# Kernel tuning notes

Measured on AMD Instinct MI355X. Metric: run time of the kernel, lower is better.

The kernel has to match this reference:

```python
import jax, jax.numpy as jnp
import numpy as np

NB, H = 4, 16
EPS = 1e-5


def _ln(x, w=None, b=None):
    m = jnp.mean(x, -1, keepdims=True)
    v = jnp.var(x, -1, keepdims=True)
    y = (x - m) * jax.lax.rsqrt(v + EPS)
    if w is not None:
        y = y * w
    if b is not None:
        y = y + b
    return y


def _ada_ln(a, s, ln_s_w, w_gamma, w_beta):
    # AF3 Algorithm 26: a <- sigmoid(Lin(LN_nobias(s))) * LN_noaffine(a) + Lin(LN_nobias(s))
    a_n = _ln(a)
    s_n = _ln(s, ln_s_w)
    return jax.nn.sigmoid(s_n @ w_gamma) * a_n + s_n @ w_beta


def setup_inputs():
    key = jax.random.key(0)
    B, S, c_a, c_s, c_z = 1, 1024, 768, 384, 128
    n_hidden = 2 * c_a  # expansion factor n=2
    ks = iter(jax.random.split(key, 40))

    def rn(shape, scale=1.0):
        return scale * jax.random.normal(next(ks), shape, dtype=jnp.float32)

    p = 0.02
    return {
        "a": rn((B, S, c_a)),
        "s": rn((B, S, c_s)),
        "z": rn((B, S, S, c_z)),
        "beta": rn((B, S, S, H)),
        # per-block AttentionPairBias params (stacked over NB blocks)
        "ln_s_w_attn": jnp.ones((NB, c_s)),
        "wg_attn": rn((NB, c_s, c_a), p),
        "wb_attn": rn((NB, c_s, c_a), p),
        "wq": rn((NB, c_a, c_a), p),
        "bq": jnp.zeros((NB, c_a)),
        "wk": rn((NB, c_a, c_a), p),
        "wv": rn((NB, c_a, c_a), p),
        "ln_z_w": jnp.ones((NB, c_z)),
        "ln_z_b": jnp.zeros((NB, c_z)),
        "wpb": rn((NB, c_z, H), p),
        "wgate": rn((NB, c_a, c_a), p),
        "wo": rn((NB, c_a, c_a), p),
        "wsg_attn": rn((NB, c_s, c_a), p),
        "bsg_attn": -2.0 * jnp.ones((NB, c_a)),
        # per-block ConditionedTransitionBlock params
        "ln_s_w_tr": jnp.ones((NB, c_s)),
        "wg_tr": rn((NB, c_s, c_a), p),
        "wb_tr": rn((NB, c_s, c_a), p),
        "w_swish": rn((NB, c_a, n_hidden), p),
        "w_gate2": rn((NB, c_a, n_hidden), p),
        "wsg_tr": rn((NB, c_s, c_a), p),
        "bsg_tr": -2.0 * jnp.ones((NB, c_a)),
        "w_out": rn((NB, n_hidden, c_a), p),
    }


def reference(a, s, z, beta, ln_s_w_attn, wg_attn, wb_attn, wq, bq, wk, wv,
              ln_z_w, ln_z_b, wpb, wgate, wo, wsg_attn, bsg_attn,
              ln_s_w_tr, wg_tr, wb_tr, w_swish, w_gate2, wsg_tr, bsg_tr, w_out):
    B, S, c_a = a.shape
    d = c_a // H
    scale = 1.0 / jnp.sqrt(jnp.float32(d))
    for i in range(NB):
        # --- AttentionPairBias (AF3 Alg 24) ---
        ah = _ada_ln(a, s, ln_s_w_attn[i], wg_attn[i], wb_attn[i])
        q = (ah @ wq[i] + bq[i]).reshape(B, S, H, d)
        k = (ah @ wk[i]).reshape(B, S, H, d)
        v = (ah @ wv[i]).reshape(B, S, H, d)
        zb = _ln(z, ln_z_w[i], ln_z_b[i]) @ wpb[i]  # [B,S,S,H] pair bias
        scores = jnp.einsum('bihd,bjhd->bhij', q, k) * scale \
                 + jnp.transpose(zb + beta, (0, 3, 1, 2))
        attn = jax.nn.softmax(scores, axis=-1)
        o = jnp.einsum('bhij,bjhd->bihd', attn, v)
        g = jax.nn.sigmoid(ah @ wgate[i]).reshape(B, S, H, d)
        att_out = (g * o).reshape(B, S, c_a) @ wo[i]
        b_attn = jax.nn.sigmoid(s @ wsg_attn[i] + bsg_attn[i]) * att_out
        # --- ConditionedTransitionBlock (AF3 Alg 25, SwiGLU) ---
        th = _ada_ln(a, s, ln_s_w_tr[i], wg_tr[i], wb_tr[i])
        hidden = jax.nn.silu(th @ w_swish[i]) * (th @ w_gate2[i])
        tr = jax.nn.sigmoid(s @ wsg_tr[i] + bsg_tr[i]) * (hidden @ w_out[i])
        a = b_attn + tr
    return a
```

## Files before the change

kernel.cpp:

```cpp
#include <hip/hip_runtime.h>
#include <hip/hip_bf16.h>

typedef __hip_bfloat16 bf16;
typedef __attribute__((ext_vector_type(8))) short s8v;
typedef __attribute__((ext_vector_type(4))) float f4v;

constexpr int S = 1024, CA = 768, CS = 384, CZ = 128, NHID = 1536;
constexpr int NBLK = 4, NHEAD = 16, DH = 48;
constexpr float EPS = 1e-5f;

#define DEV static __device__ __forceinline__

DEV float sigmoidf_(float x) { return 1.0f / (1.0f + __expf(-x)); }

DEV f4v mfma16(s8v a, s8v b, f4v c) {
  return __builtin_amdgcn_mfma_f32_16x16x32_bf16(a, b, c, 0, 0, 0);
}

union U8 { s8v s; bf16 h[8]; };
union U4 { uint2 u; bf16 h[4]; };

DEV float wred_sum(float v) {
#pragma unroll
  for (int o = 32; o; o >>= 1) v += __shfl_xor(v, o);
  return v;
}

struct PrepFatArgs {
  const float* tsrc[14];
  bf16* tdst[14];
  const float* tcs[14];
  long tdstZ[14];
  const float *ln_z_w, *ln_z_b, *wpb, *bq, *bsg_a, *bsg_t;
  bf16* W2T; float* bias2; float* biasQKVG; float* biasSG;
  const float* s_in; bf16* s_hat; bf16* s_bf;
};

__global__ __launch_bounds__(256) void prep_fat(PrepFatArgs a) {
  __shared__ __align__(16) float tile[1056];
  const int bid = blockIdx.x, t = threadIdx.x;
  if (bid < 32256) {
    int ti, blk, x, y, K, N;
    if (bid < 6912) {
      const int lb = bid; ti = lb / 1152; const int r2 = lb % 1152;
      blk = r2 / 288; const int rem = r2 % 288; x = rem % 24; y = rem / 24; K = 384; N = 768;
    } else if (bid < 18432) {
      const int lb = bid - 6912; ti = 6 + lb / 2304; const int r2 = lb % 2304;
      blk = r2 / 576; const int rem = r2 % 576; x = rem % 24; y = rem / 24; K = 768; N = 768;
    } else if (bid < 27648) {
      const int lb = bid - 18432; ti = 11 + lb / 4608; const int r2 = lb % 4608;
      blk = r2 / 1152; const int rem = r2 % 1152; x = rem % 48; y = rem / 48; K = 768; N = 1536;
    } else {
      const int lb = bid - 27648; ti = 13; blk = lb / 1152;
      const int rem = lb % 1152; x = rem % 24; y = rem / 24; K = 1536; N = 768;
    }
    const float* src = a.tsrc[ti] + (size_t)blk * K * N;
    bf16* dst = a.tdst[ti] + (size_t)blk * a.tdstZ[ti];
    const float* cs = a.tcs[ti] ? (a.tcs[ti] + blk * CS) : nullptr;
    const int k0 = y * 32, n0 = x * 32, tx = t & 31, ty = t >> 5;
#pragma unroll
    for (int q = 0; q < 4; ++q) {
      const int k = k0 + ty + 8 * q;
      float v = src[(size_t)k * N + n0 + tx];
      if (cs) v *= cs[k];
      tile[(ty + 8 * q) * 33 + tx] = v;
    }
    __syncthreads();
#pragma unroll
    for (int q = 0; q < 4; ++q)
      dst[(size_t)(n0 + ty + 8 * q) * K + k0 + tx] = __float2bfloat16(tile[tx * 33 + ty + 8 * q]);
    return;
  }
  if (bid < 32305) {
    const int pid = bid - 32256;
    if (pid == 48) {
      for (int f = t; f < 64 * CZ; f += 256) {
        const int col = f >> 7, c = f & 127, b = col >> 4, h = col & 15;
        a.W2T[f] = __float2bfloat16(a.ln_z_w[b * CZ + c] * a.wpb[(b * CZ + c) * NHEAD + h]);
      }
      if (t < 64) {
        const int b = t >> 4, h = t & 15;
        float sum = 0.f;
        for (int c = 0; c < CZ; ++c)
          sum += a.ln_z_b[b * CZ + c] * a.wpb[(b * CZ + c) * NHEAD + h];
        a.bias2[t] = sum;
      }
      return;
    }
    const int g = pid * 256 + t;
    if (g < 4 * 3072) {
      const int b = g / 3072, c = g % 3072;
      a.biasQKVG[g] = (c < 768) ? a.bq[b * 768 + c] : 0.f;
    }
    if (g < 6144) {
      const int b = g / 1536, c = g % 1536;
      a.biasSG[g] = (c < 768) ? a.bsg_a[b * 768 + c] : a.bsg_t[b * 768 + c - 768];
    }
    return;
  }
  {
    float* red = tile;
    const size_t row = bid - 32305;
    float4 v = make_float4(0.f, 0.f, 0.f, 0.f);
    if (t < CS / 4) v = ((const float4*)(a.s_in + row * CS))[t];
    float sum = v.x + v.y + v.z + v.w;
    float sq = v.x * v.x + v.y * v.y + v.z * v.z + v.w * v.w;
    sum = wred_sum(sum); sq = wred_sum(sq);
    const int wv = t >> 6;
    if ((t & 63) == 0) { red[2 * wv] = sum; red[2 * wv + 1] = sq; }
    __syncthreads();
    sum = red[0] + red[2] + red[4] + red[6];
    sq = red[1] + red[3] + red[5] + red[7];
    const float m = sum / CS;
    const float rstd = rsqrtf(sq / CS - m * m + EPS);
    if (t < CS / 4) {
      U4 oh, ob_;
      oh.h[0] = __float2bfloat16((v.x - m) * rstd); oh.h[1] = __float2bfloat16((v.y - m) * rstd);
      oh.h[2] = __float2bfloat16((v.z - m) * rstd); oh.h[3] = __float2bfloat16((v.w - m) * rstd);
      ob_.h[0] = __float2bfloat16(v.x); ob_.h[1] = __float2bfloat16(v.y);
      ob_.h[2] = __float2bfloat16(v.z); ob_.h[3] = __float2bfloat16(v.w);
      *(uint2*)(a.s_hat + row * CS + 4 * t) = oh.u;
      *(uint2*)(a.s_bf + row * CS + 4 * t) = ob_.u;
    }
  }
}

__global__ __launch_bounds__(256) void ln_adaln2(const float* __restrict__ a,
                                                 const bf16* __restrict__ ada,
                                                 bf16* __restrict__ ah_attn,
                                                 bf16* __restrict__ ah_tr) {
  __shared__ float red[8];
  const int t = threadIdx.x;
  const size_t row = blockIdx.x;
  float4 v = make_float4(0.f, 0.f, 0.f, 0.f);
  if (t < 192) v = ((const float4*)(a + row * CA))[t];
  float sum = v.x + v.y + v.z + v.w;
  float sq = v.x * v.x + v.y * v.y + v.z * v.z + v.w * v.w;
  sum = wred_sum(sum); sq = wred_sum(sq);
  const int wv = t >> 6;
  if ((t & 63) == 0) { red[2 * wv] = sum; red[2 * wv + 1] = sq; }
  __syncthreads();
  sum = red[0] + red[2] + red[4] + red[6];
  sq = red[1] + red[3] + red[5] + red[7];
  const float m = sum / CA;
  const float rstd = rsqrtf(sq / CA - m * m + EPS);
  if (t < 192) {
    const float an[4] = {(v.x - m) * rstd, (v.y - m) * rstd, (v.z - m) * rstd, (v.w - m) * rstd};
    const bf16* ar = ada + row * 12288 + 4 * t;
    U4 g1, b1, g2, b2, o1, o2;
    g1.u = *(const uint2*)(ar);
    b1.u = *(const uint2*)(ar + 768);
    g2.u = *(const uint2*)(ar + 1536);
    b2.u = *(const uint2*)(ar + 2304);
#pragma unroll
    for (int j = 0; j < 4; ++j) {
      o1.h[j] = __float2bfloat16(sigmoidf_(__bfloat162float(g1.h[j])) * an[j] + __bfloat162float(b1.h[j]));
      o2.h[j] = __float2bfloat16(sigmoidf_(__bfloat162float(g2.h[j])) * an[j] + __bfloat162float(b2.h[j]));
    }
    *(uint2*)(ah_attn + row * CA + 4 * t) = o1.u;
    *(uint2*)(ah_tr + row * CA + 4 * t) = o2.u;
  }
}

__global__ __launch_bounds__(256) void final_adaln(const float* __restrict__ sg,
                                                   const bf16* __restrict__ att,
                                                   const bf16* __restrict__ tr,
                                                   const bf16* __restrict__ ada,
                                                   bf16* __restrict__ ah_attn,
                                                   bf16* __restrict__ ah_tr) {
  __shared__ float red[8];
  const int t = threadIdx.x;
  const size_t row = blockIdx.x;
  float o[4] = {0.f, 0.f, 0.f, 0.f};
  if (t < 192) {
    const float4 sa = *(const float4*)(sg + row * 6144 + 4 * t);
    const float4 st = *(const float4*)(sg + row * 6144 + 768 + 4 * t);
    U4 av, tv;
    av.u = *(const uint2*)(att + row * CA + 4 * t);
    tv.u = *(const uint2*)(tr + row * CA + 4 * t);
    o[0] = sa.x * __bfloat162float(av.h[0]) + st.x * __bfloat162float(tv.h[0]);
    o[1] = sa.y * __bfloat162float(av.h[1]) + st.y * __bfloat162float(tv.h[1]);
    o[2] = sa.z * __bfloat162float(av.h[2]) + st.z * __bfloat162float(tv.h[2]);
    o[3] = sa.w * __bfloat162float(av.h[3]) + st.w * __bfloat162float(tv.h[3]);
  }
  float sum = o[0] + o[1] + o[2] + o[3];
  float sq = o[0] * o[0] + o[1] * o[1] + o[2] * o[2] + o[3] * o[3];
  sum = wred_sum(sum); sq = wred_sum(sq);
  const int wv = t >> 6;
  if ((t & 63) == 0) { red[2 * wv] = sum; red[2 * wv + 1] = sq; }
  __syncthreads();
  sum = red[0] + red[2] + red[4] + red[6];
  sq = red[1] + red[3] + red[5] + red[7];
  const float m = sum / CA;
  const float rstd = rsqrtf(sq / CA - m * m + EPS);
  if (t < 192) {
    const bf16* ar = ada + row * 12288 + 4 * t;
    U4 g1, b1, g2, b2, o1, o2;
    g1.u = *(const uint2*)(ar);
    b1.u = *(const uint2*)(ar + 768);
    g2.u = *(const uint2*)(ar + 1536);
    b2.u = *(const uint2*)(ar + 2304);
#pragma unroll
    for (int j = 0; j < 4; ++j) {
      const float an = (o[j] - m) * rstd;
      o1.h[j] = __float2bfloat16(sigmoidf_(__bfloat162float(g1.h[j])) * an + __bfloat162float(b1.h[j]));
      o2.h[j] = __float2bfloat16(sigmoidf_(__bfloat162float(g2.h[j])) * an + __bfloat162float(b2.h[j]));
    }
    *(uint2*)(ah_attn + row * CA + 4 * t) = o1.u;
    *(uint2*)(ah_tr + row * CA + 4 * t) = o2.u;
  }
}

__global__ __launch_bounds__(256) void ew_final(const float* __restrict__ sg,
                                                const bf16* __restrict__ att,
                                                const bf16* __restrict__ tr,
                                                float* __restrict__ out) {
  const int i = blockIdx.x * 256 + threadIdx.x;
  const int row = i / 192, col = (i % 192) * 4;
  const float4 sa = *(const float4*)(sg + (size_t)row * 6144 + col);
  const float4 st = *(const float4*)(sg + (size_t)row * 6144 + 768 + col);
  U4 av, tv;
  av.u = *(const uint2*)(att + (size_t)row * CA + col);
  tv.u = *(const uint2*)(tr + (size_t)row * CA + col);
  float4 o;
  o.x = sa.x * __bfloat162float(av.h[0]) + st.x * __bfloat162float(tv.h[0]);
  o.y = sa.y * __bfloat162float(av.h[1]) + st.y * __bfloat162float(tv.h[1]);
  o.z = sa.z * __bfloat162float(av.h[2]) + st.z * __bfloat162float(tv.h[2]);
  o.w = sa.w * __bfloat162float(av.h[3]) + st.w * __bfloat162float(tv.h[3]);
  *(float4*)(out + (size_t)row * CA + col) = o;
}

__global__ __launch_bounds__(256) void zbias_kernel(const float* __restrict__ z,
                                                    const float* __restrict__ beta,
                                                    const bf16* __restrict__ W2T,
                                                    const float* __restrict__ bias2,
                                                    bf16* __restrict__ bias_all) {
  __shared__ s8v zt8[64 * 16];
  __shared__ s8v w2s[64 * 16];
  __shared__ float betas[64][17];
  __shared__ float bias2s[64];
  __shared__ bf16 obuf[64][72];
  const int t = threadIdx.x;
  const int i = blockIdx.y, j0 = blockIdx.x * 64;
#pragma unroll
  for (int q = 0; q < 4; ++q) {
    const int u = q * 256 + t;
    const int row = u >> 4, sl = u & 15;
    w2s[row * 16 + (sl ^ (row & 7))] = *(const s8v*)(W2T + row * CZ + sl * 8);
  }
  if (t < 64) bias2s[t] = bias2[t];
  {
    const int j = t >> 2, h4 = t & 3;
    const float4 bv = *(const float4*)(beta + ((size_t)i * S + j0 + j) * NHEAD + 4 * h4);
    betas[j][4 * h4 + 0] = bv.x; betas[j][4 * h4 + 1] = bv.y;
    betas[j][4 * h4 + 2] = bv.z; betas[j][4 * h4 + 3] = bv.w;
  }
  {
    const int p = t >> 2, q = t & 3;
    const float* zr = z + ((size_t)i * S + j0 + p) * CZ + q * 32;
    float vals[32];
    float sum = 0.f, sq = 0.f;
#pragma unroll
    for (int k4 = 0; k4 < 8; ++k4) {
      const float4 xv = *(const float4*)(zr + 4 * k4);
      vals[4 * k4 + 0] = xv.x; vals[4 * k4 + 1] = xv.y;
      vals[4 * k4 + 2] = xv.z; vals[4 * k4 + 3] = xv.w;
      sum += xv.x + xv.y + xv.z + xv.w;
      sq += xv.x * xv.x + xv.y * xv.y + xv.z * xv.z + xv.w * xv.w;
    }
    sum += __shfl_xor(sum, 1); sum += __shfl_xor(sum, 2);
    sq += __shfl_xor(sq, 1); sq += __shfl_xor(sq, 2);
    const float m = sum / CZ;
    const float rstd = rsqrtf(sq / CZ - m * m + EPS);
#pragma unroll
    for (int u = 0; u < 4; ++u) {
      U8 pk;
#pragma unroll
      for (int e = 0; e < 8; ++e) pk.h[e] = __float2bfloat16((vals[8 * u + e] - m) * rstd);
      const int cu = 4 * q + u;
      zt8[p * 16 + (cu ^ (p & 7))] = pk.s;
    }
  }
  __syncthreads();
  const int lane = t & 63, wid = t >> 6;
  const int wr = wid >> 1, wc = wid & 1;
  const int ln = lane & 15, lq = lane >> 4;
  f4v acc[2][2] = {};
#pragma unroll
  for (int kk = 0; kk < 4; ++kk) {
    const int sl = (lq + 4 * kk) ^ (ln & 7);
    s8v a[2], b[2];
#pragma unroll
    for (int mi = 0; mi < 2; ++mi) a[mi] = zt8[(32 * wr + 16 * mi + ln) * 16 + sl];
#pragma unroll
    for (int ni = 0; ni < 2; ++ni) b[ni] = w2s[(32 * wc + 16 * ni + ln) * 16 + sl];
#pragma unroll
    for (int mi = 0; mi < 2; ++mi)
#pragma unroll
      for (int ni = 0; ni < 2; ++ni) acc[mi][ni] = mfma16(a[mi], b[ni], acc[mi][ni]);
  }
#pragma unroll
  for (int mi = 0; mi < 2; ++mi)
#pragma unroll
    for (int ni = 0; ni < 2; ++ni) {
      const int col = 32 * wc + 16 * ni + ln;
      const int jb = 32 * wr + 16 * mi + 4 * lq;
      U4 o4;
#pragma unroll
      for (int r = 0; r < 4; ++r)
        o4.h[r] = __float2bfloat16(acc[mi][ni][r] + bias2s[col] + betas[jb + r][col & 15]);
      *(uint2*)&obuf[col][jb] = o4.u;
    }
  __syncthreads();
  {
    const int oc = t >> 2, js = (t & 3) * 16;
    bf16* dp = bias_all + (size_t)oc * S * S + (size_t)i * S + j0 + js;
    *(s8v*)dp = *(const s8v*)&obuf[oc][js];
    *(s8v*)(dp + 8) = *(const s8v*)&obuf[oc][js + 8];
  }
}

struct GemmAArgs {
  const bf16* A0[2]; int lda0[2];
  const bf16* A1[2]; int lda1[2];
  const bf16* Bt[2];
  const float* bias[2];
  void* C[2];
  int K[2]; int N[2]; int nb[2];
  int amode[2]; int outMode[2];
  bf16* vT;
};

DEV s8v combineRT(s8v x, s8v y, int amode) {
  U8 ux, uy, rr;
  ux.s = x; uy.s = y;
#pragma unroll
  for (int j = 0; j < 8; ++j) {
    const float fx = __bfloat162float(ux.h[j]);
    const float fy = __bfloat162float(uy.h[j]);
    const float tt = sigmoidf_(fx);
    rr.h[j] = __float2bfloat16((amode == 2 ? fx * tt : tt) * fy);
  }
  return rr.s;
}

__global__ __launch_bounds__(256) void gemmA(GemmAArgs ga) {
  const int z = blockIdx.z;
  if ((int)blockIdx.x >= ga.nb[z]) return;
  __shared__ s8v As[512];
  __shared__ s8v Bs[1024];
  const bf16* A0 = ga.A0[z]; const int lda0 = ga.lda0[z];
  const bf16* A1 = ga.A1[z]; const int lda1 = ga.lda1[z];
  const bf16* Bt = ga.Bt[z];
  const float* bias = ga.bias[z];
  const int K = ga.K[z], N = ga.N[z], amode = ga.amode[z], om = ga.outMode[z];
  const int t = threadIdx.x;
  const int lane = t & 63, wid = t >> 6;
  const int wr = wid >> 1, wc = wid & 1;
  const int ln = lane & 15, lq = lane >> 4;
  const int m0 = blockIdx.y * 64, n0 = blockIdx.x * 128;
  int rowA[2], slA[2], swzA[2];
#pragma unroll
  for (int q = 0; q < 2; ++q) {
    const int u = q * 256 + t;
    rowA[q] = u >> 3; slA[q] = u & 7;
    swzA[q] = rowA[q] * 8 + (slA[q] ^ (rowA[q] & 7));
  }
  int rowB[4], slB[4], swzB[4];
#pragma unroll
  for (int q = 0; q < 4; ++q) {
    const int u = q * 256 + t;
    rowB[q] = u >> 3; slB[q] = u & 7;
    swzB[q] = rowB[q] * 8 + (slB[q] ^ (rowB[q] & 7));
  }
  f4v acc[2][4] = {};
  s8v ra[2], ra2[2], rb[4];
#pragma unroll
  for (int q = 0; q < 2; ++q) {
    ra[q] = *(const s8v*)(A0 + (size_t)(m0 + rowA[q]) * lda0 + slA[q] * 8);
    if (amode != 0) ra2[q] = *(const s8v*)(A1 + (size_t)(m0 + rowA[q]) * lda1 + slA[q] * 8);
  }
#pragma unroll
  for (int q = 0; q < 4; ++q)
    rb[q] = *(const s8v*)(Bt + (size_t)(n0 + rowB[q]) * K + slB[q] * 8);
  for (int ks = 0;;) {
    __syncthreads();
#pragma unroll
    for (int q = 0; q < 2; ++q)
      As[swzA[q]] = (amode == 0) ? ra[q] : combineRT(ra[q], ra2[q], amode);
#pragma unroll
    for (int q = 0; q < 4; ++q) Bs[swzB[q]] = rb[q];
    const int ksn = ks + 64;
    if (ksn < K) {
#pragma unroll
      for (int q = 0; q < 2; ++q) {
        ra[q] = *(const s8v*)(A0 + (size_t)(m0 + rowA[q]) * lda0 + ksn + slA[q] * 8);
        if (amode != 0) ra2[q] = *(const s8v*)(A1 + (size_t)(m0 + rowA[q]) * lda1 + ksn + slA[q] * 8);
      }
#pragma unroll
      for (int q = 0; q < 4; ++q)
        rb[q] = *(const s8v*)(Bt + (size_t)(n0 + rowB[q]) * K + ksn + slB[q] * 8);
    }
    __syncthreads();
#pragma unroll
    for (int kk = 0; kk < 2; ++kk) {
      const int sl = (lq + 4 * kk) ^ (ln & 7);
      s8v a[2], b[4];
#pragma unroll
      for (int mi = 0; mi < 2; ++mi) a[mi] = As[(32 * wr + 16 * mi + ln) * 8 + sl];
#pragma unroll
      for (int ni = 0; ni < 4; ++ni) b[ni] = Bs[(64 * wc + 16 * ni + ln) * 8 + sl];
#pragma unroll
      for (int mi = 0; mi < 2; ++mi)
#pragma unroll
        for (int ni = 0; ni < 4; ++ni) acc[mi][ni] = mfma16(a[mi], b[ni], acc[mi][ni]);
    }
    ks = ksn;
    if (ks >= K) break;
  }
  const bool vdiv = (ga.vT != nullptr) && (z == 0) && (n0 >= 1536) && (n0 < 2304);
#pragma unroll
  for (int ni = 0; ni < 4; ++ni) {
    const int n = n0 + 64 * wc + 16 * ni + ln;
    const float bv = bias ? bias[n] : 0.f;
#pragma unroll
    for (int mi = 0; mi < 2; ++mi) {
      const int mb = m0 + 32 * wr + 16 * mi + 4 * lq;
      if (vdiv) {
        U4 o4;
#pragma unroll
        for (int r = 0; r < 4; ++r) o4.h[r] = __float2bfloat16(acc[mi][ni][r] + bv);
        *(uint2*)(ga.vT + (size_t)(n - 1536) * S + mb) = o4.u;
      } else if (om == 0) {
        bf16* Cb = (bf16*)ga.C[z];
#pragma unroll
        for (int r = 0; r < 4; ++r)
          Cb[(size_t)(mb + r) * N + n] = __float2bfloat16(acc[mi][ni][r] + bv);
      } else {
        float* Cf = (float*)ga.C[z];
#pragma unroll
        for (int r = 0; r < 4; ++r)
          Cf[(size_t)(mb + r) * N + n] = sigmoidf_(acc[mi][ni][r] + bv);
      }
    }
  }
}

__global__ __launch_bounds__(256) void flash_split(const bf16* __restrict__ qkvg,
                                                   const bf16* __restrict__ vT,
                                                   const bf16* __restrict__ bias_all,
                                                   float* __restrict__ opart,
                                                   float* __restrict__ ml, int blk) {
  __shared__ s8v Qs[64 * 8];
  __shared__ s8v Ks[64 * 8];
  __shared__ s8v Vs[48 * 8];
  __shared__ s8v Bs[64 * 8];
  __shared__ bf16 PwB[4 * 1024];
  __shared__ float facL[4][16];
  const int t = threadIdx.x;
  const int lane = t & 63, w = t >> 6;
  const int ln = lane & 15, lq = lane >> 4;
  const int h = blockIdx.y, i0 = blockIdx.x * 64, part = blockIdx.z;
  const bf16* bp = bias_all + (size_t)(blk * NHEAD + h) * S * S;
  const float scale = 0.14433756729740643f;

#pragma unroll
  for (int uu = 0; uu < 2; ++uu) {
    const int u = t + 256 * uu, row = u >> 3, sl = u & 7;
    s8v qv{};
    if (sl < 6) qv = *(const s8v*)(qkvg + (size_t)(i0 + row) * 3072 + h * DH + sl * 8);
    Qs[row * 8 + (sl ^ (row & 7))] = qv;
  }

  s8v kr[2], br[2], vr0{}, vr1{};
  auto prefetch = [&](int jt) {
    const int j0 = jt * 64;
#pragma unroll
    for (int uu = 0; uu < 2; ++uu) {
      const int u = t + 256 * uu, row = u >> 3, sl = u & 7;
      s8v kv{};
      if (sl < 6) kv = *(const s8v*)(qkvg + (size_t)(j0 + row) * 3072 + 768 + h * DH + sl * 8);
      kr[uu] = kv;
      br[uu] = *(const s8v*)(bp + (size_t)(i0 + row) * S + j0 + sl * 8);
    }
    { const int d = t >> 3, sl = t & 7;
      vr0 = *(const s8v*)(vT + (size_t)(h * DH + d) * S + j0 + sl * 8); }
    if (t < 128) {
      const int u = 256 + t, d = u >> 3, sl = u & 7;
      vr1 = *(const s8v*)(vT + (size_t)(h * DH + d) * S + j0 + sl * 8);
    }
  };
  auto store_tiles = [&]() {
#pragma unroll
    for (int uu = 0; uu < 2; ++uu) {
      const int u = t + 256 * uu, row = u >> 3, sl = u & 7;
      const int ph = row * 8 + (sl ^ (row & 7));
      Ks[ph] = kr[uu];
      Bs[ph] = br[uu];
    }
    { const int d = t >> 3, sl = t & 7;
      Vs[d * 8 + (sl ^ (d & 7))] = vr0; }
    if (t < 128) {
      const int u = 256 + t, d = u >> 3, sl = u & 7;
      Vs[d * 8 + (sl ^ (d & 7))] = vr1;
    }
  };

  float m_run = -3e30f, l_run = 0.f;
  f4v acc_o[3] = {};
  bf16* pw = PwB + w * 1024;

  prefetch(part * 4);
  for (int jt2 = 0; jt2 < 4; ++jt2) {
    __syncthreads();
    store_tiles();
    __syncthreads();
    if (jt2 < 3) prefetch(part * 4 + jt2 + 1);
    float p[4][4];
    float tmax = -3e30f;
    __builtin_amdgcn_s_setprio(1);
#pragma unroll
    for (int ja = 0; ja < 4; ++ja) {
      f4v accs = {};
#pragma unroll
      for (int ks2 = 0; ks2 < 2; ++ks2) {
        const int sl = (lq + 4 * ks2) ^ (ln & 7);
        const s8v a = Ks[(16 * ja + ln) * 8 + sl];
        const s8v b = Qs[(16 * w + ln) * 8 + sl];
        accs = mfma16(a, b, accs);
      }
      const int jq = 4 * ja + lq;
      const int pu = jq >> 1;
      U4 bv;
      bv.u = *(const uint2*)((const bf16*)(&Bs[0]) +
                             (((16 * w + ln) * 8 + (pu ^ (ln & 7))) * 8 + (jq & 1) * 4));
#pragma unroll
      for (int r = 0; r < 4; ++r) {
        p[ja][r] = accs[r] * scale + __bfloat162float(bv.h[r]);
        tmax = fmaxf(tmax, p[ja][r]);
      }
    }
    __builtin_amdgcn_s_setprio(0);
    tmax = fmaxf(tmax, __shfl_xor(tmax, 16));
    tmax = fmaxf(tmax, __shfl_xor(tmax, 32));
    const float m_new = fmaxf(m_run, tmax);
    const float fac = __expf(m_run - m_new);
    m_run = m_new;
    float psum = 0.f;
#pragma unroll
    for (int ja = 0; ja < 4; ++ja)
#pragma unroll
      for (int r = 0; r < 4; ++r) {
        p[ja][r] = __expf(p[ja][r] - m_new);
        psum += p[ja][r];
      }
    psum += __shfl_xor(psum, 16);
    psum += __shfl_xor(psum, 32);
    l_run = l_run * fac + psum;
    if (lq == 0) facL[w][ln] = fac;
#pragma unroll
    for (int ja = 0; ja < 4; ++ja) {
      const int ju = 4 * ja + lq;
      const int ph = ju ^ ((ln & 7) << 1);
      U4 pk;
#pragma unroll
      for (int r = 0; r < 4; ++r) pk.h[r] = __float2bfloat16(p[ja][r]);
      *(uint2*)(pw + ln * 64 + ph * 4) = pk.u;
    }
    asm volatile("s_waitcnt lgkmcnt(0)" ::: "memory");
    __builtin_amdgcn_sched_barrier(0);
    const float4 fv = *(const float4*)&facL[w][4 * lq];
#pragma unroll
    for (int ni = 0; ni < 3; ++ni) {
      acc_o[ni][0] *= fv.x; acc_o[ni][1] *= fv.y;
      acc_o[ni][2] *= fv.z; acc_o[ni][3] *= fv.w;
    }
    __builtin_amdgcn_s_setprio(1);
#pragma unroll
    for (int ks2 = 0; ks2 < 2; ++ks2) {
      const int pu0 = (2 * lq + 8 * ks2) ^ ((ln & 7) << 1);
      const s8v pa = *(const s8v*)(pw + ln * 64 + pu0 * 4);
      const int slv = (lq + 4 * ks2) ^ (ln & 7);
#pragma unroll
      for (int ni = 0; ni < 3; ++ni) {
        const s8v vb = Vs[(16 * ni + ln) * 8 + slv];
        acc_o[ni] = mfma16(pa, vb, acc_o[ni]);
      }
    }
    __builtin_amdgcn_s_setprio(0);
  }
  if (lq == 0) {
    ((float2*)ml)[(size_t)(part * NHEAD + h) * S + i0 + 16 * w + ln] =
        make_float2(m_run, l_run);
  }
  float* op = opart + (size_t)part * S * CA;
#pragma unroll
  for (int ni = 0; ni < 3; ++ni)
#pragma unroll
    for (int r = 0; r < 4; ++r) {
      const int m = i0 + 16 * w + 4 * lq + r;
      op[(size_t)m * CA + h * DH + 16 * ni + ln] = acc_o[ni][r];
    }
}

__global__ __launch_bounds__(256) void flash_combine4(const float* __restrict__ opart,
                                                      const float* __restrict__ ml,
                                                      const bf16* __restrict__ gate,
                                                      bf16* __restrict__ go) {
  const int row = blockIdx.x, t = threadIdx.x;
  if (t >= 192) return;
  const int c = 4 * t, h = t / 12;
  const float2* mlp = (const float2*)ml;
  const float2 a0 = mlp[(size_t)(0 * NHEAD + h) * S + row];
  const float2 a1 = mlp[(size_t)(1 * NHEAD + h) * S + row];
  const float2 a2 = mlp[(size_t)(2 * NHEAD + h) * S + row];
  const float2 a3 = mlp[(size_t)(3 * NHEAD + h) * S + row];
  const float M = fmaxf(fmaxf(a0.x, a1.x), fmaxf(a2.x, a3.x));
  const float w0 = __expf(a0.x - M), w1 = __expf(a1.x - M);
  const float w2 = __expf(a2.x - M), w3 = __expf(a3.x - M);
  const float inv = 1.0f / (w0 * a0.y + w1 * a1.y + w2 * a2.y + w3 * a3.y);
  const size_t rc = (size_t)row * CA + c;
  const float4 o0 = *(const float4*)(opart + rc);
  const float4 o1 = *(const float4*)(opart + (size_t)S * CA + rc);
  const float4 o2 = *(const float4*)(opart + (size_t)2 * S * CA + rc);
  const float4 o3 = *(const float4*)(opart + (size_t)3 * S * CA + rc);
  U4 g;
  g.u = *(const uint2*)(gate + (size_t)row * 3072 + c);
  U4 o;
  o.h[0] = __float2bfloat16(sigmoidf_(__bfloat162float(g.h[0])) *
                            ((w0 * o0.x + w1 * o1.x + w2 * o2.x + w3 * o3.x) * inv));
  o.h[1] = __float2bfloat16(sigmoidf_(__bfloat162float(g.h[1])) *
                            ((w0 * o0.y + w1 * o1.y + w2 * o2.y + w3 * o3.y) * inv));
  o.h[2] = __float2bfloat16(sigmoidf_(__bfloat162float(g.h[2])) *
                            ((w0 * o0.z + w1 * o1.z + w2 * o2.z + w3 * o3.z) * inv));
  o.h[3] = __float2bfloat16(sigmoidf_(__bfloat162float(g.h[3])) *
                            ((w0 * o0.w + w1 * o1.w + w2 * o2.w + w3 * o3.w) * inv));
  *(uint2*)(go + (size_t)row * CA + c) = o.u;
}

__global__ void fill_kernel(float* p, int n, float v) {
  const int i = blockIdx.x * 256 + threadIdx.x;
  if (i < n) p[i] = v;
}

extern "C" void kernel_launch(void* const* d_in, const int* in_sizes, int n_in,
                              void* d_out, int out_size, void* d_ws, size_t ws_size,
                              hipStream_t stream) {
  (void)in_sizes; (void)n_in;
  const float* a_in = (const float*)d_in[0];
  const float* s_in = (const float*)d_in[1];
  const float* z_in = (const float*)d_in[2];
  const float* beta = (const float*)d_in[3];
  const float* ln_s_w_attn = (const float*)d_in[4];
  const float* wg_attn = (const float*)d_in[5];
  const float* wb_attn = (const float*)d_in[6];
  const float* wq = (const float*)d_in[7];
  const float* bq = (const float*)d_in[8];
  const float* wk = (const float*)d_in[9];
  const float* wv = (const float*)d_in[10];
  const float* ln_z_w = (const float*)d_in[11];
  const float* ln_z_b = (const float*)d_in[12];
  const float* wpb = (const float*)d_in[13];
  const float* wgate = (const float*)d_in[14];
  const float* wo = (const float*)d_in[15];
  const float* wsg_attn = (const float*)d_in[16];
  const float* bsg_attn = (const float*)d_in[17];
  const float* ln_s_w_tr = (const float*)d_in[18];
  const float* wg_tr = (const float*)d_in[19];
  const float* wb_tr = (const float*)d_in[20];
  const float* w_swish = (const float*)d_in[21];
  const float* w_gate2 = (const float*)d_in[22];
  const float* wsg_tr = (const float*)d_in[23];
  const float* bsg_tr = (const float*)d_in[24];
  const float* w_out = (const float*)d_in[25];

  char* wp = (char*)d_ws;
  size_t used = 0;
  auto alloc = [&](size_t bytes) -> void* {
    void* p = wp + used;
    used += (bytes + 255) & ~(size_t)255;
    return p;
  };
  bf16* bias_all = (bf16*)alloc((size_t)64 * S * S * 2);
  bf16* WT_ada = (bf16*)alloc((size_t)4 * 3072 * 384 * 2);
  bf16* WT_sg = (bf16*)alloc((size_t)4 * 1536 * 384 * 2);
  bf16* WT_qkvg = (bf16*)alloc((size_t)4 * 3072 * 768 * 2);
  bf16* WT_wo = (bf16*)alloc((size_t)4 * 768 * 768 * 2);
  bf16* WT_mlp = (bf16*)alloc((size_t)4 * 3072 * 768 * 2);
  bf16* WT_wout = (bf16*)alloc((size_t)4 * 768 * 1536 * 2);
  float* biasQKVG = (float*)alloc(4 * 3072 * 4);
  float* biasSG = (float*)alloc(6144 * 4);
  bf16* W2T = (bf16*)alloc(64 * 128 * 2);
  float* bias2 = (float*)alloc(64 * 4);
  bf16* ada_all = (bf16*)alloc((size_t)S * 12288 * 2);
  float* sg_all = (float*)alloc((size_t)S * 6144 * 4);
  bf16* s_hat = (bf16*)alloc((size_t)S * CS * 2);
  bf16* s_bf = (bf16*)alloc((size_t)S * CS * 2);
  bf16* ah_attn = (bf16*)alloc((size_t)S * CA * 2);
  bf16* ah_tr = (bf16*)alloc((size_t)S * CA * 2);
  bf16* qkvg = (bf16*)alloc((size_t)S * 3072 * 2);
  bf16* vT = (bf16*)alloc((size_t)CA * S * 2);
  bf16* go = (bf16*)alloc((size_t)S * CA * 2);
  bf16* att = (bf16*)alloc((size_t)S * CA * 2);
  bf16* swg = (bf16*)alloc((size_t)S * 3072 * 2);
  bf16* trout = (bf16*)alloc((size_t)S * CA * 2);
  float* opart = (float*)alloc((size_t)4 * S * CA * 4);
  float* ml = (float*)alloc((size_t)4 * NHEAD * S * 8);
  if (used > ws_size) {
    fill_kernel<<<(out_size + 255) / 256, 256, 0, stream>>>((float*)d_out, out_size, 12345.0f);
    return;
  }

  const dim3 B256(256);

  {
    PrepFatArgs pa{};
    pa.tsrc[0] = wg_attn;  pa.tdst[0] = WT_ada + (size_t)0 * 384;    pa.tcs[0] = ln_s_w_attn; pa.tdstZ[0] = 3072 * 384;
    pa.tsrc[1] = wb_attn;  pa.tdst[1] = WT_ada + (size_t)768 * 384;  pa.tcs[1] = ln_s_w_attn; pa.tdstZ[1] = 3072 * 384;
    pa.tsrc[2] = wg_tr;    pa.tdst[2] = WT_ada + (size_t)1536 * 384; pa.tcs[2] = ln_s_w_tr;   pa.tdstZ[2] = 3072 * 384;
    pa.tsrc[3] = wb_tr;    pa.tdst[3] = WT_ada + (size_t)2304 * 384; pa.tcs[3] = ln_s_w_tr;   pa.tdstZ[3] = 3072 * 384;
    pa.tsrc[4] = wsg_attn; pa.tdst[4] = WT_sg + (size_t)0 * 384;     pa.tcs[4] = nullptr;     pa.tdstZ[4] = 1536 * 384;
    pa.tsrc[5] = wsg_tr;   pa.tdst[5] = WT_sg + (size_t)768 * 384;   pa.tcs[5] = nullptr;     pa.tdstZ[5] = 1536 * 384;
    pa.tsrc[6] = wq;    pa.tdst[6] = WT_qkvg + (size_t)0 * 768;    pa.tdstZ[6] = 3072 * 768;
    pa.tsrc[7] = wk;    pa.tdst[7] = WT_qkvg + (size_t)768 * 768;  pa.tdstZ[7] = 3072 * 768;
    pa.tsrc[8] = wv;    pa.tdst[8] = WT_qkvg + (size_t)1536 * 768; pa.tdstZ[8] = 3072 * 768;
    pa.tsrc[9] = wgate; pa.tdst[9] = WT_qkvg + (size_t)2304 * 768; pa.tdstZ[9] = 3072 * 768;
    pa.tsrc[10] = wo;   pa.tdst[10] = WT_wo;                       pa.tdstZ[10] = 768 * 768;
    pa.tsrc[11] = w_swish; pa.tdst[11] = WT_mlp + (size_t)0 * 768;    pa.tdstZ[11] = 3072 * 768;
    pa.tsrc[12] = w_gate2; pa.tdst[12] = WT_mlp + (size_t)1536 * 768; pa.tdstZ[12] = 3072 * 768;
    pa.tsrc[13] = w_out; pa.tdst[13] = WT_wout; pa.tdstZ[13] = 768 * 1536;
    pa.ln_z_w = ln_z_w; pa.ln_z_b = ln_z_b; pa.wpb = wpb;
    pa.bq = bq; pa.bsg_a = bsg_attn; pa.bsg_t = bsg_tr;
    pa.W2T = W2T; pa.bias2 = bias2; pa.biasQKVG = biasQKVG; pa.biasSG = biasSG;
    pa.s_in = s_in; pa.s_hat = s_hat; pa.s_bf = s_bf;
    prep_fat<<<33329, B256, 0, stream>>>(pa);
  }

  zbias_kernel<<<dim3(16, 1024), B256, 0, stream>>>(z_in, beta, W2T, bias2, bias_all);

  {
    GemmAArgs ga{};
    ga.A0[0] = s_hat; ga.lda0[0] = 384; ga.Bt[0] = WT_ada; ga.bias[0] = nullptr;
    ga.C[0] = ada_all; ga.K[0] = 384; ga.N[0] = 12288; ga.nb[0] = 96;
    ga.amode[0] = 0; ga.outMode[0] = 0;
    ga.A0[1] = s_bf; ga.lda0[1] = 384; ga.Bt[1] = WT_sg; ga.bias[1] = biasSG;
    ga.C[1] = sg_all; ga.K[1] = 384; ga.N[1] = 6144; ga.nb[1] = 48;
    ga.amode[1] = 0; ga.outMode[1] = 1;
    ga.vT = nullptr;
    gemmA<<<dim3(96, 16, 2), B256, 0, stream>>>(ga);
  }

  ln_adaln2<<<S, B256, 0, stream>>>(a_in, ada_all, ah_attn, ah_tr);
  for (int b = 0; b < NBLK; ++b) {
    {
      GemmAArgs ga{};
      ga.A0[0] = ah_attn; ga.lda0[0] = 768; ga.Bt[0] = WT_qkvg + (size_t)b * 3072 * 768;
      ga.bias[0] = biasQKVG + b * 3072; ga.C[0] = qkvg; ga.K[0] = 768; ga.N[0] = 3072;
      ga.nb[0] = 24; ga.amode[0] = 0; ga.outMode[0] = 0;
      ga.A0[1] = ah_tr; ga.lda0[1] = 768; ga.Bt[1] = WT_mlp + (size_t)b * 3072 * 768;
      ga.bias[1] = nullptr; ga.C[1] = swg; ga.K[1] = 768; ga.N[1] = 3072;
      ga.nb[1] = 24; ga.amode[1] = 0; ga.outMode[1] = 0;
      ga.vT = vT;
      gemmA<<<dim3(24, 16, 2), B256, 0, stream>>>(ga);
    }
    flash_split<<<dim3(16, 16, 4), B256, 0, stream>>>(qkvg, vT, bias_all, opart, ml, b);
    flash_combine4<<<S, B256, 0, stream>>>(opart, ml, qkvg + 2304, go);
    {
      GemmAArgs ga{};
      ga.A0[0] = go; ga.lda0[0] = 768;
      ga.Bt[0] = WT_wo + (size_t)b * 768 * 768; ga.bias[0] = nullptr;
      ga.C[0] = att; ga.K[0] = 768; ga.N[0] = 768; ga.nb[0] = 6;
      ga.amode[0] = 0; ga.outMode[0] = 0;
      ga.A0[1] = swg; ga.lda0[1] = 3072; ga.A1[1] = swg + 1536; ga.lda1[1] = 3072;
      ga.Bt[1] = WT_wout + (size_t)b * 768 * 1536; ga.bias[1] = nullptr;
      ga.C[1] = trout; ga.K[1] = 1536; ga.N[1] = 768; ga.nb[1] = 6;
      ga.amode[1] = 2; ga.outMode[1] = 0;
      ga.vT = nullptr;
      gemmA<<<dim3(6, 16, 2), B256, 0, stream>>>(ga);
    }
    if (b < NBLK - 1) {
      final_adaln<<<S, B256, 0, stream>>>(sg_all + (size_t)b * 1536, att, trout,
                                          ada_all + (size_t)(b + 1) * 3072, ah_attn, ah_tr);
    } else {
      ew_final<<<768, B256, 0, stream>>>(sg_all + (size_t)b * 1536, att, trout, (float*)d_out);
    }
  }
}
```

Baseline: 581.5 us.

## Fuse flash split-combine and gating into output-projection GEMM; halve KV splits

Splits the flash attention key range into 2 parts instead of 4, so each block processes 8 key tiles, and double-buffers the K/V/bias LDS tiles. The separate flash_combine4 kernel is removed. The output-projection GEMM now merges the two partial outputs and applies the sigmoid gate while loading its A tiles (amode 3). This removes one launch, the go intermediate and half of the partial-output traffic. In exchange the flash grid is half the size, and the A operand of the projection GEMM is loaded synchronously with scalar fp32 reads and recomputed by each of the 6 N-blocks.

```diff
diff --git a/kernel.cpp b/kernel.cpp
--- a/kernel.cpp
+++ b/kernel.cpp
@@ -329,6 +329,9 @@
   int K[2]; int N[2]; int nb[2];
   int amode[2]; int outMode[2];
   bf16* vT;
+  const float* opA;
+  const float* mlA;
+  const bf16* gateA;
 };
 
 DEV s8v combineRT(s8v x, s8v y, int amode) {
@@ -342,6 +345,26 @@
     rr.h[j] = __float2bfloat16((amode == 2 ? fx * tt : tt) * fy);
   }
   return rr.s;
+}
+
+DEV s8v combineFlash(const float* opart, const float* ml, const bf16* gate,
+                     int row, int k) {
+  const int h = k / DH;
+  const float2 m1 = ((const float2*)ml)[(size_t)h * S + row];
+  const float2 m2 = ((const float2*)ml)[(size_t)(NHEAD + h) * S + row];
+  const float M = fmaxf(m1.x, m2.x);
+  const float w1 = __expf(m1.x - M), w2 = __expf(m2.x - M);
+  const float inv = 1.0f / (w1 * m1.y + w2 * m2.y);
+  const float* o1p = opart + (size_t)row * CA + k;
+  const float* o2p = opart + (size_t)S * CA + (size_t)row * CA + k;
+  U8 g; g.s = *(const s8v*)(gate + (size_t)row * 3072 + k);
+  U8 r;
+#pragma unroll
+  for (int j = 0; j < 8; ++j) {
+    const float v = (w1 * o1p[j] + w2 * o2p[j]) * inv;
+    r.h[j] = __float2bfloat16(sigmoidf_(__bfloat162float(g.h[j])) * v);
+  }
+  return r.s;
 }
 
 __global__ __launch_bounds__(256) void gemmA(GemmAArgs ga) {
@@ -375,27 +398,37 @@
   }
   f4v acc[2][4] = {};
   s8v ra[2], ra2[2], rb[4];
-#pragma unroll
-  for (int q = 0; q < 2; ++q) {
-    ra[q] = *(const s8v*)(A0 + (size_t)(m0 + rowA[q]) * lda0 + slA[q] * 8);
-    if (amode != 0) ra2[q] = *(const s8v*)(A1 + (size_t)(m0 + rowA[q]) * lda1 + slA[q] * 8);
+  if (amode != 3) {
+#pragma unroll
+    for (int q = 0; q < 2; ++q) {
+      ra[q] = *(const s8v*)(A0 + (size_t)(m0 + rowA[q]) * lda0 + slA[q] * 8);
+      if (amode != 0) ra2[q] = *(const s8v*)(A1 + (size_t)(m0 + rowA[q]) * lda1 + slA[q] * 8);
+    }
   }
 #pragma unroll
   for (int q = 0; q < 4; ++q)
     rb[q] = *(const s8v*)(Bt + (size_t)(n0 + rowB[q]) * K + slB[q] * 8);
   for (int ks = 0;;) {
     __syncthreads();
-#pragma unroll
-    for (int q = 0; q < 2; ++q)
-      As[swzA[q]] = (amode == 0) ? ra[q] : combineRT(ra[q], ra2[q], amode);
+    if (amode == 3) {
+#pragma unroll
+      for (int q = 0; q < 2; ++q)
+        As[swzA[q]] = combineFlash(ga.opA, ga.mlA, ga.gateA, m0 + rowA[q], ks + slA[q] * 8);
+    } else {
+#pragma unroll
+      for (int q = 0; q < 2; ++q)
+        As[swzA[q]] = (amode == 0) ? ra[q] : combineRT(ra[q], ra2[q], amode);
+    }
 #pragma unroll
     for (int q = 0; q < 4; ++q) Bs[swzB[q]] = rb[q];
     const int ksn = ks + 64;
     if (ksn < K) {
-#pragma unroll
-      for (int q = 0; q < 2; ++q) {
-        ra[q] = *(const s8v*)(A0 + (size_t)(m0 + rowA[q]) * lda0 + ksn + slA[q] * 8);
-        if (amode != 0) ra2[q] = *(const s8v*)(A1 + (size_t)(m0 + rowA[q]) * lda1 + ksn + slA[q] * 8);
+      if (amode != 3) {
+#pragma unroll
+        for (int q = 0; q < 2; ++q) {
+          ra[q] = *(const s8v*)(A0 + (size_t)(m0 + rowA[q]) * lda0 + ksn + slA[q] * 8);
+          if (amode != 0) ra2[q] = *(const s8v*)(A1 + (size_t)(m0 + rowA[q]) * lda1 + ksn + slA[q] * 8);
+        }
       }
 #pragma unroll
       for (int q = 0; q < 4; ++q)
@@ -452,15 +485,15 @@
                                                    float* __restrict__ opart,
                                                    float* __restrict__ ml, int blk) {
   __shared__ s8v Qs[64 * 8];
-  __shared__ s8v Ks[64 * 8];
-  __shared__ s8v Vs[48 * 8];
-  __shared__ s8v Bs[64 * 8];
+  __shared__ s8v Ks[2][64 * 8];
+  __shared__ s8v Vs[2][48 * 8];
+  __shared__ s8v Bs[2][64 * 8];
   __shared__ bf16 PwB[4 * 1024];
   __shared__ float facL[4][16];
   const int t = threadIdx.x;
   const int lane = t & 63, w = t >> 6;
   const int ln = lane & 15, lq = lane >> 4;
-  const int h = blockIdx.y, i0 = blockIdx.x * 64, part = blockIdx.z;
+  const int h = blockIdx.y, i0 = blockIdx.x * 64, half = blockIdx.z;
   const bf16* bp = bias_all + (size_t)(blk * NHEAD + h) * S * S;
   const float scale = 0.14433756729740643f;
 
@@ -490,19 +523,19 @@
       vr1 = *(const s8v*)(vT + (size_t)(h * DH + d) * S + j0 + sl * 8);
     }
   };
-  auto store_tiles = [&]() {
+  auto store_tiles = [&](int pb) {
 #pragma unroll
     for (int uu = 0; uu < 2; ++uu) {
       const int u = t + 256 * uu, row = u >> 3, sl = u & 7;
       const int ph = row * 8 + (sl ^ (row & 7));
-      Ks[ph] = kr[uu];
-      Bs[ph] = br[uu];
+      Ks[pb][ph] = kr[uu];
+      Bs[pb][ph] = br[uu];
     }
     { const int d = t >> 3, sl = t & 7;
-      Vs[d * 8 + (sl ^ (d & 7))] = vr0; }
+      Vs[pb][d * 8 + (sl ^ (d & 7))] = vr0; }
     if (t < 128) {
       const int u = 256 + t, d = u >> 3, sl = u & 7;
-      Vs[d * 8 + (sl ^ (d & 7))] = vr1;
+      Vs[pb][d * 8 + (sl ^ (d & 7))] = vr1;
     }
   };
 
@@ -510,12 +543,13 @@
   f4v acc_o[3] = {};
   bf16* pw = PwB + w * 1024;
 
-  prefetch(part * 4);
-  for (int jt2 = 0; jt2 < 4; ++jt2) {
+  prefetch(half * 8);
+  for (int jt2 = 0; jt2 < 8; ++jt2) {
+    const int pb = jt2 & 1;
     __syncthreads();
-    store_tiles();
+    store_tiles(pb);
     __syncthreads();
-    if (jt2 < 3) prefetch(part * 4 + jt2 + 1);
+    if (jt2 < 7) prefetch(half * 8 + jt2 + 1);
     float p[4][4];
     float tmax = -3e30f;
     __builtin_amdgcn_s_setprio(1);
@@ -525,14 +559,14 @@
 #pragma unroll
       for (int ks2 = 0; ks2 < 2; ++ks2) {
         const int sl = (lq + 4 * ks2) ^ (ln & 7);
-        const s8v a = Ks[(16 * ja + ln) * 8 + sl];
+        const s8v a = Ks[pb][(16 * ja + ln) * 8 + sl];
         const s8v b = Qs[(16 * w + ln) * 8 + sl];
         accs = mfma16(a, b, accs);
       }
       const int jq = 4 * ja + lq;
       const int pu = jq >> 1;
       U4 bv;
-      bv.u = *(const uint2*)((const bf16*)(&Bs[0]) +
+      bv.u = *(const uint2*)((const bf16*)(&Bs[pb][0]) +
                              (((16 * w + ln) * 8 + (pu ^ (ln & 7))) * 8 + (jq & 1) * 4));
 #pragma unroll
       for (int r = 0; r < 4; ++r) {
@@ -583,17 +617,17 @@
       const int slv = (lq + 4 * ks2) ^ (ln & 7);
 #pragma unroll
       for (int ni = 0; ni < 3; ++ni) {
-        const s8v vb = Vs[(16 * ni + ln) * 8 + slv];
+        const s8v vb = Vs[pb][(16 * ni + ln) * 8 + slv];
         acc_o[ni] = mfma16(pa, vb, acc_o[ni]);
       }
     }
     __builtin_amdgcn_s_setprio(0);
   }
   if (lq == 0) {
-    ((float2*)ml)[(size_t)(part * NHEAD + h) * S + i0 + 16 * w + ln] =
+    ((float2*)ml)[(size_t)(half * NHEAD + h) * S + i0 + 16 * w + ln] =
         make_float2(m_run, l_run);
   }
-  float* op = opart + (size_t)part * S * CA;
+  float* op = opart + (size_t)half * S * CA;
 #pragma unroll
   for (int ni = 0; ni < 3; ++ni)
 #pragma unroll
@@ -601,41 +635,6 @@
       const int m = i0 + 16 * w + 4 * lq + r;
       op[(size_t)m * CA + h * DH + 16 * ni + ln] = acc_o[ni][r];
     }
-}
-
-__global__ __launch_bounds__(256) void flash_combine4(const float* __restrict__ opart,
-                                                      const float* __restrict__ ml,
-                                                      const bf16* __restrict__ gate,
-                                                      bf16* __restrict__ go) {
-  const int row = blockIdx.x, t = threadIdx.x;
-  if (t >= 192) return;
-  const int c = 4 * t, h = t / 12;
-  const float2* mlp = (const float2*)ml;
-  const float2 a0 = mlp[(size_t)(0 * NHEAD + h) * S + row];
-  const float2 a1 = mlp[(size_t)(1 * NHEAD + h) * S + row];
-  const float2 a2 = mlp[(size_t)(2 * NHEAD + h) * S + row];
-  const float2 a3 = mlp[(size_t)(3 * NHEAD + h) * S + row];
-  const float M = fmaxf(fmaxf(a0.x, a1.x), fmaxf(a2.x, a3.x));
-  const float w0 = __expf(a0.x - M), w1 = __expf(a1.x - M);
-  const float w2 = __expf(a2.x - M), w3 = __expf(a3.x - M);
-  const float inv = 1.0f / (w0 * a0.y + w1 * a1.y + w2 * a2.y + w3 * a3.y);
-  const size_t rc = (size_t)row * CA + c;
-  const float4 o0 = *(const float4*)(opart + rc);
-  const float4 o1 = *(const float4*)(opart + (size_t)S * CA + rc);
-  const float4 o2 = *(const float4*)(opart + (size_t)2 * S * CA + rc);
-  const float4 o3 = *(const float4*)(opart + (size_t)3 * S * CA + rc);
-  U4 g;
-  g.u = *(const uint2*)(gate + (size_t)row * 3072 + c);
-  U4 o;
-  o.h[0] = __float2bfloat16(sigmoidf_(__bfloat162float(g.h[0])) *
-                            ((w0 * o0.x + w1 * o1.x + w2 * o2.x + w3 * o3.x) * inv));
-  o.h[1] = __float2bfloat16(sigmoidf_(__bfloat162float(g.h[1])) *
-                            ((w0 * o0.y + w1 * o1.y + w2 * o2.y + w3 * o3.y) * inv));
-  o.h[2] = __float2bfloat16(sigmoidf_(__bfloat162float(g.h[2])) *
-                            ((w0 * o0.z + w1 * o1.z + w2 * o2.z + w3 * o3.z) * inv));
-  o.h[3] = __float2bfloat16(sigmoidf_(__bfloat162float(g.h[3])) *
-                            ((w0 * o0.w + w1 * o1.w + w2 * o2.w + w3 * o3.w) * inv));
-  *(uint2*)(go + (size_t)row * CA + c) = o.u;
 }
 
 __global__ void fill_kernel(float* p, int n, float v) {
@@ -700,12 +699,11 @@
   bf16* ah_tr = (bf16*)alloc((size_t)S * CA * 2);
   bf16* qkvg = (bf16*)alloc((size_t)S * 3072 * 2);
   bf16* vT = (bf16*)alloc((size_t)CA * S * 2);
-  bf16* go = (bf16*)alloc((size_t)S * CA * 2);
   bf16* att = (bf16*)alloc((size_t)S * CA * 2);
   bf16* swg = (bf16*)alloc((size_t)S * 3072 * 2);
   bf16* trout = (bf16*)alloc((size_t)S * CA * 2);
-  float* opart = (float*)alloc((size_t)4 * S * CA * 4);
-  float* ml = (float*)alloc((size_t)4 * NHEAD * S * 8);
+  float* opart = (float*)alloc((size_t)2 * S * CA * 4);
+  float* ml = (float*)alloc((size_t)2 * NHEAD * S * 8);
   if (used > ws_size) {
     fill_kernel<<<(out_size + 255) / 256, 256, 0, stream>>>((float*)d_out, out_size, 12345.0f);
     return;
@@ -763,19 +761,19 @@
       ga.vT = vT;
       gemmA<<<dim3(24, 16, 2), B256, 0, stream>>>(ga);
     }
-    flash_split<<<dim3(16, 16, 4), B256, 0, stream>>>(qkvg, vT, bias_all, opart, ml, b);
-    flash_combine4<<<S, B256, 0, stream>>>(opart, ml, qkvg + 2304, go);
+    flash_split<<<dim3(16, 16, 2), B256, 0, stream>>>(qkvg, vT, bias_all, opart, ml, b);
     {
       GemmAArgs ga{};
-      ga.A0[0] = go; ga.lda0[0] = 768;
+      ga.A0[0] = nullptr; ga.lda0[0] = 0;
       ga.Bt[0] = WT_wo + (size_t)b * 768 * 768; ga.bias[0] = nullptr;
       ga.C[0] = att; ga.K[0] = 768; ga.N[0] = 768; ga.nb[0] = 6;
-      ga.amode[0] = 0; ga.outMode[0] = 0;
+      ga.amode[0] = 3; ga.outMode[0] = 0;
       ga.A0[1] = swg; ga.lda0[1] = 3072; ga.A1[1] = swg + 1536; ga.lda1[1] = 3072;
       ga.Bt[1] = WT_wout + (size_t)b * 768 * 1536; ga.bias[1] = nullptr;
       ga.C[1] = trout; ga.K[1] = 1536; ga.N[1] = 768; ga.nb[1] = 6;
       ga.amode[1] = 2; ga.outMode[1] = 0;
       ga.vT = nullptr;
+      ga.opA = opart; ga.mlA = ml; ga.gateA = qkvg + 2304;
       gemmA<<<dim3(6, 16, 2), B256, 0, stream>>>(ga);
     }
     if (b < NBLK - 1) {
```

Measured after the change: 542.3 us, median of 3. 1.07x faster.
